# Kernel optimization log

Hardware: AMD Instinct MI355X
Metric: run time of the kernel (lower is better)

The kernel has to match this reference:

```python
import jax, jax.numpy as jnp
import numpy as np

B, N, H = 32, 1024, 512
THR = 0.05  # peak_detection_threshold


def _l2norm(x):
    return x / jnp.linalg.norm(x, axis=-1, keepdims=True)


def setup_inputs() -> dict:
    key = jax.random.key(0)
    ks = jax.random.split(key, 6)
    def w(k, shape, fan_in):
        return jax.random.normal(k, shape, jnp.float32) / np.float32(np.sqrt(fan_in))
    return {
        "segment_rep": jax.random.normal(ks[0], (B, N, H), jnp.float32),
        "phn_mask": jnp.ones((B, N), jnp.float32),
        # SegmentSimilarityMeasure: Linear(2H->H), ReLU, Linear(H->1, no bias)
        "W1": w(ks[1], (2 * H, H), 2 * H),
        "b1": jnp.zeros((H,), jnp.float32),
        "W2": w(ks[2], (H, 1), H),
        # word_enc: Linear(H->H), ReLU, Linear(H->H)
        "We1": w(ks[3], (H, H), H),
        "be1": jnp.zeros((H,), jnp.float32),
        "We2": w(ks[4], (H, H), H),
        "be2": jnp.zeros((H,), jnp.float32),
    }


def _forward(segment_rep, phn_mask, W1, b1, W2, We1, be1, We2, be2):
    Bs, Np, Hd = segment_rep.shape
    # adjacent segment similarity: MLP on concat of l2-normalized neighbors -> (B, N-1)
    cat = jnp.concatenate([_l2norm(segment_rep[:, :-1, :]), _l2norm(segment_rep[:, 1:, :])], axis=2)
    S = (jax.nn.relu(cat @ W1 + b1) @ W2)[..., 0]

    # relative dissimilarity
    Smin = jnp.min(S, axis=1, keepdims=True)
    Smax = jnp.max(S, axis=1, keepdims=True)
    D = 1.0 - (S - Smin) / (Smax - Smin)

    # peak detector (faithful to original, incl. final overwrite of first-order cols -2:)
    z = jnp.zeros_like(D)
    fo = z
    fo = fo.at[:, 0].set(jnp.maximum(D[:, 0] - D[:, 1], 0.0))
    fo = fo.at[:, 1:-1].set(jnp.minimum(jnp.maximum(D[:, 1:-1] - D[:, :-2], 0.0),
                                        jnp.maximum(D[:, 1:-1] - D[:, 2:], 0.0)))
    fo = fo.at[:, -1].set(jnp.maximum(D[:, -1] - D[:, -2], 0.0))
    so = z
    so = so.at[:, 0:2].set(jnp.maximum(D[:, 0:2] - D[:, 2:4], 0.0))
    so = so.at[:, 2:-2].set(jnp.minimum(jnp.maximum(D[:, 2:-2] - D[:, :-4], 0.0),
                                        jnp.maximum(D[:, 2:-2] - D[:, 4:], 0.0)))
    fo = fo.at[:, -2:].set(jnp.maximum(D[:, -2:] - D[:, -4:-2], 0.0))  # replicates original code
    P = jnp.minimum(jnp.maximum(jnp.maximum(fo, so) - THR, 0.0), fo)

    # pad, mask, straight-through hard boundaries
    P = jnp.pad(P, ((0, 0), (0, 1)))
    P = jax.nn.relu(P + (phn_mask - 1.0))
    b_soft = jnp.tanh(10.0 * P)
    b_hard = jnp.tanh(100000.0 * P)
    b = b_soft + jax.lax.stop_gradient(b_hard - b_soft)
    b = jnp.cumsum(b, axis=1)  # (B, N)
    b = b + (b[:, :1] == 0).astype(b.dtype)  # per-row +1 if b[:,0]==0
    num_word_segments = b[:, -1].astype(jnp.int32) + 1  # (B,)

    # U: column j holds j+1 for j < num_word_segments[i], else -100000. Nmax = N (static bound).
    cols = jnp.arange(1, Np + 1, dtype=jnp.int32)  # (Nmax,)
    U = jnp.where(cols[None, :] <= num_word_segments[:, None],
                  cols.astype(segment_rep.dtype)[None, :], -100000.0)  # (B, Nmax)

    V = U[:, None, :] - b[:, :, None]  # (B, N, Nmax)
    Wseg = 1.0 - jnp.tanh(100000.0 * jnp.abs(V))
    Wseg = Wseg / jnp.sum(Wseg, axis=1, keepdims=True)
    Wseg = jnp.nan_to_num(Wseg)

    # pool: (B, Nmax, N) @ (B, N, H) -> (B, Nmax, H)
    word_rep = jnp.einsum('bnm,bnh->bmh', Wseg, segment_rep)
    word_masks = jnp.where(word_rep == 0, 0.0, 1.0)
    out = jax.nn.relu(word_rep @ We1 + be1) @ We2 + be2
    return out * word_masks


def reference(segment_rep, phn_mask, W1, b1, W2, We1, be1, We2, be2):
    return _forward(segment_rep, phn_mask, W1, b1, W2, We1, be1, We2, be2)
```

## Files before the change

kernel.cpp:

```cpp
#include <hip/hip_runtime.h>

#define BB 32
#define NN 1024
#define HH 512
#define NS 1023

typedef unsigned short u16;
typedef unsigned int   u32;
typedef __attribute__((ext_vector_type(8))) short bf16x8;
typedef __attribute__((ext_vector_type(4))) float f32x4;

__device__ __forceinline__ float bf2f(u16 h) {
  union { u32 u; float f; } c; c.u = ((u32)h) << 16; return c.f;
}
__device__ __forceinline__ u16 f2bf(float f) {
  union { float f; u32 u; } c; c.f = f;
  u32 u = c.u;
  return (u16)((u + 0x7fffu + ((u >> 16) & 1u)) >> 16);
}
__device__ __forceinline__ void split_bf(float x, u16& hi, u16& lo) {
  hi = f2bf(x);
  lo = f2bf(x - bf2f(hi));
}
__device__ __forceinline__ void dma16(const u16* g, u16* l) {
  __builtin_amdgcn_global_load_lds(
      (const __attribute__((address_space(1))) u32*)g,
      (__attribute__((address_space(3))) u32*)l, 16, 0, 0);
}

__global__ __launch_bounds__(64) void k_prep_a(const float* __restrict__ seg,
                                               u16* __restrict__ ahi,
                                               u16* __restrict__ alo) {
  int row = blockIdx.x, lane = threadIdx.x;
  const float4* p = (const float4*)(seg + ((size_t)row << 9) + lane * 8);
  float4 a = p[0], b = p[1];
  float v[8] = {a.x, a.y, a.z, a.w, b.x, b.y, b.z, b.w};
  float s = 0.f;
#pragma unroll
  for (int i = 0; i < 8; ++i) s += v[i] * v[i];
#pragma unroll
  for (int m = 32; m; m >>= 1) s += __shfl_xor(s, m, 64);
  float nrm = sqrtf(s);
  u16 h[8], l[8];
#pragma unroll
  for (int i = 0; i < 8; ++i) split_bf(v[i] / nrm, h[i], l[i]);
  size_t off = ((size_t)row << 9) + lane * 8;
  *(uint4*)(ahi + off) = make_uint4(h[0] | (h[1] << 16), h[2] | (h[3] << 16),
                                    h[4] | (h[5] << 16), h[6] | (h[7] << 16));
  *(uint4*)(alo + off) = make_uint4(l[0] | (l[1] << 16), l[2] | (l[3] << 16),
                                    l[4] | (l[5] << 16), l[6] | (l[7] << 16));
}

__global__ __launch_bounds__(256) void k_tr(const float* __restrict__ src,
                                            u16* __restrict__ dh,
                                            u16* __restrict__ dl,
                                            int K, int N) {
  __shared__ u16 Th[64 * 66], Tl[64 * 66];
  int nb = blockIdx.x * 64, kb = blockIdx.y * 64;
  int tid = threadIdx.x;
#pragma unroll
  for (int i = 0; i < 16; ++i) {
    int e = tid + i * 256;
    int r = e >> 6, c = e & 63;
    float v = src[(size_t)(kb + r) * N + nb + c];
    u16 hi, lo; split_bf(v, hi, lo);
    Th[c * 66 + r] = hi;
    Tl[c * 66 + r] = lo;
  }
  __syncthreads();
#pragma unroll
  for (int i = 0; i < 16; ++i) {
    int e = tid + i * 256;
    int n = e >> 6, k = e & 63;
    dh[(size_t)(nb + n) * K + kb + k] = Th[n * 66 + k];
    if (dl) dl[(size_t)(nb + n) * K + kb + k] = Tl[n * 66 + k];
  }
}

__global__ __launch_bounds__(512, 2) void k_sgemm(const u16* __restrict__ ahi,
                                                  const u16* __restrict__ alo,
                                                  const u16* __restrict__ w1h,
                                                  const u16* __restrict__ w1l,
                                                  const float* __restrict__ b1,
                                                  const float* __restrict__ W2,
                                                  float* __restrict__ Spart) {
  __shared__ u16 Ah[2][256 * 32];
  __shared__ u16 Al[2][256 * 32];
  __shared__ u16 Bh[2][256 * 32];
  __shared__ u16 Bl[2][256 * 32];

  const int tid  = threadIdx.x;
  const int wave = tid >> 6, lane = tid & 63;
  const int quad = lane >> 4, l15 = lane & 15;
  const int wm = wave >> 2, wn = wave & 3;
  const int r_in = lane >> 2, c_in = lane & 3;
  const int nblk = blockIdx.x, mblk = blockIdx.y;
  const int mrow0 = mblk * 256;
  const int ncol0 = nblk * 256;

#define SG_A(g_, tb_, ks_)                                                   \
  {                                                                          \
    int k0_ = (ks_) * 32, half_ = k0_ >> 9, cb_ = k0_ & 511;                 \
    int grow_ = mrow0 + wave * 32 + (g_) * 16 + r_in + half_;                \
    if (grow_ > 32767) grow_ = 32767;                                        \
    size_t ga_ = (((size_t)grow_) << 9) + cb_ + c_in * 8;                    \
    dma16(ahi + ga_, &Ah[tb_][(wave * 32 + (g_) * 16) * 32]);                \
    dma16(alo + ga_, &Al[tb_][(wave * 32 + (g_) * 16) * 32]);                \
  }
#define SG_B(g_, tb_, ks_)                                                   \
  {                                                                          \
    int k0_ = (ks_) * 32;                                                    \
    int n_ = ncol0 + wave * 32 + (g_) * 16 + r_in;                           \
    size_t gb_ = (((size_t)n_) << 10) + k0_ + c_in * 8;                      \
    dma16(w1h + gb_, &Bh[tb_][(wave * 32 + (g_) * 16) * 32]);                \
    dma16(w1l + gb_, &Bl[tb_][(wave * 32 + (g_) * 16) * 32]);                \
  }

  f32x4 acc[8][4];
#pragma unroll
  for (int mi = 0; mi < 8; ++mi)
#pragma unroll
    for (int ni = 0; ni < 4; ++ni) acc[mi][ni] = (f32x4){0.f, 0.f, 0.f, 0.f};

  SG_A(0, 0, 0) SG_A(1, 0, 0) SG_B(0, 0, 0) SG_B(1, 0, 0)
  asm volatile("s_waitcnt vmcnt(0)" ::: "memory");
  __builtin_amdgcn_s_barrier();

  for (int ks = 0; ks < 32; ++ks) {
    const int bb = ks & 1;
    const bool pre = (ks + 1) < 32;
    bf16x8 ah[8], al[8], bh[4], bl[4];

#pragma unroll
    for (int mi = 0; mi < 8; ++mi)
      ah[mi] = *(const bf16x8*)&Ah[bb][(wm * 128 + mi * 16 + l15) * 32 + quad * 8];
#pragma unroll
    for (int ni = 0; ni < 4; ++ni)
      bh[ni] = *(const bf16x8*)&Bh[bb][(wn * 64 + ni * 16 + l15) * 32 + quad * 8];
    if (pre) { SG_A(0, bb ^ 1, ks + 1) SG_B(0, bb ^ 1, ks + 1) }
    __builtin_amdgcn_s_barrier();
    asm volatile("s_waitcnt lgkmcnt(0)" ::: "memory");
    __builtin_amdgcn_sched_barrier(0);
    __builtin_amdgcn_s_setprio(1);
#pragma unroll
    for (int ni = 0; ni < 4; ++ni)
#pragma unroll
      for (int mi = 0; mi < 8; ++mi)
        acc[mi][ni] = __builtin_amdgcn_mfma_f32_16x16x32_bf16(ah[mi], bh[ni], acc[mi][ni], 0, 0, 0);
    __builtin_amdgcn_s_setprio(0);
    __builtin_amdgcn_s_barrier();

#pragma unroll
    for (int ni = 0; ni < 4; ++ni)
      bl[ni] = *(const bf16x8*)&Bl[bb][(wn * 64 + ni * 16 + l15) * 32 + quad * 8];
    if (pre) { SG_A(1, bb ^ 1, ks + 1) SG_B(1, bb ^ 1, ks + 1) }
    __builtin_amdgcn_s_barrier();
    asm volatile("s_waitcnt lgkmcnt(0)" ::: "memory");
    __builtin_amdgcn_sched_barrier(0);
    __builtin_amdgcn_s_setprio(1);
#pragma unroll
    for (int ni = 0; ni < 4; ++ni)
#pragma unroll
      for (int mi = 0; mi < 8; ++mi)
        acc[mi][ni] = __builtin_amdgcn_mfma_f32_16x16x32_bf16(ah[mi], bl[ni], acc[mi][ni], 0, 0, 0);
    __builtin_amdgcn_s_setprio(0);
    __builtin_amdgcn_s_barrier();

#pragma unroll
    for (int mi = 0; mi < 8; ++mi)
      al[mi] = *(const bf16x8*)&Al[bb][(wm * 128 + mi * 16 + l15) * 32 + quad * 8];
    __builtin_amdgcn_s_barrier();
    asm volatile("s_waitcnt lgkmcnt(0)" ::: "memory");
    __builtin_amdgcn_sched_barrier(0);
    __builtin_amdgcn_s_setprio(1);
#pragma unroll
    for (int ni = 0; ni < 4; ++ni)
#pragma unroll
      for (int mi = 0; mi < 8; ++mi)
        acc[mi][ni] = __builtin_amdgcn_mfma_f32_16x16x32_bf16(al[mi], bh[ni], acc[mi][ni], 0, 0, 0);
    __builtin_amdgcn_s_setprio(0);
    asm volatile("s_waitcnt vmcnt(0)" ::: "memory");
    __builtin_amdgcn_s_barrier();
  }
#undef SG_A
#undef SG_B

  float* red = (float*)&Ah[0][0];
  float b1v[4], w2v[4];
#pragma unroll
  for (int ni = 0; ni < 4; ++ni) {
    int n_g = ncol0 + wn * 64 + ni * 16 + l15;
    b1v[ni] = b1[n_g];
    w2v[ni] = W2[n_g];
  }
#pragma unroll
  for (int mi = 0; mi < 8; ++mi) {
#pragma unroll
    for (int reg = 0; reg < 4; ++reg) {
      float part = 0.f;
#pragma unroll
      for (int ni = 0; ni < 4; ++ni) {
        float h = acc[mi][ni][reg] + b1v[ni];
        h = h > 0.f ? h : 0.f;
        part = fmaf(h, w2v[ni], part);
      }
#pragma unroll
      for (int m = 8; m; m >>= 1) part += __shfl_xor(part, m, 64);
      if (l15 == 0) red[wave * 128 + mi * 16 + quad * 4 + reg] = part;
    }
  }
  __syncthreads();
  if (tid < 256) {
    int wmr = tid >> 7, rl = tid & 127;
    float s = red[(wmr * 4 + 0) * 128 + rl] + red[(wmr * 4 + 1) * 128 + rl]
            + red[(wmr * 4 + 2) * 128 + rl] + red[(wmr * 4 + 3) * 128 + rl];
    int grow = mrow0 + tid;
    int b = grow >> 10, n = grow & 1023;
    if (n < NS)
      Spart[((size_t)nblk * BB + b) * NN + n] = s;
  }
}

__global__ __launch_bounds__(256) void k_row(const float* __restrict__ S0,
                                             const float* __restrict__ S1,
                                             const float* __restrict__ mask,
                                             int* __restrict__ assign,
                                             float* __restrict__ weight,
                                             float* __restrict__ total,
                                             int* __restrict__ startn,
                                             int* __restrict__ endn) {
  int b = blockIdx.x, tid = threadIdx.x;
  __shared__ float Ssh[NS];
  __shared__ float Dsh[NS];
  __shared__ float tsh[NN];
  __shared__ float bsh[NN];
  __shared__ float totl[NN];
  __shared__ int   stl[NN];
  __shared__ int   enl[NN];
  __shared__ float red[256];

  for (int n = tid; n < NS; n += 256)
    Ssh[n] = S0[((size_t)b << 10) + n] + S1[((size_t)b << 10) + n];
  __syncthreads();

  float mn = INFINITY, mx = -INFINITY;
  for (int n = tid; n < NS; n += 256) {
    float v = Ssh[n];
    mn = fminf(mn, v); mx = fmaxf(mx, v);
  }
  red[tid] = mn; __syncthreads();
  for (int s = 128; s; s >>= 1) { if (tid < s) red[tid] = fminf(red[tid], red[tid + s]); __syncthreads(); }
  float Smin = red[0]; __syncthreads();
  red[tid] = mx; __syncthreads();
  for (int s = 128; s; s >>= 1) { if (tid < s) red[tid] = fmaxf(red[tid], red[tid + s]); __syncthreads(); }
  float Smax = red[0]; __syncthreads();

  for (int n = tid; n < NS; n += 256)
    Dsh[n] = 1.0f - (Ssh[n] - Smin) / (Smax - Smin);
  __syncthreads();

  for (int n = tid; n < NN; n += 256) {
    float P;
    if (n >= NS) {
      P = 0.f;
    } else {
      float D = Dsh[n];
      float fo, so;
      if (n == 0)            fo = fmaxf(D - Dsh[1], 0.f);
      else if (n >= NS - 2)  fo = fmaxf(D - Dsh[n - 2], 0.f);
      else                   fo = fminf(fmaxf(D - Dsh[n - 1], 0.f),
                                        fmaxf(D - Dsh[n + 1], 0.f));
      if (n <= 1)            so = fmaxf(D - Dsh[n + 2], 0.f);
      else if (n >= NS - 2)  so = 0.f;
      else                   so = fminf(fmaxf(D - Dsh[n - 2], 0.f),
                                        fmaxf(D - Dsh[n + 2], 0.f));
      P = fminf(fmaxf(fmaxf(fo, so) - 0.05f, 0.f), fo);
    }
    float m = mask[((size_t)b << 10) + n];
    P = P + (m - 1.0f);
    P = P > 0.f ? P : 0.f;
    float bs = tanhf(10.0f * P);
    float bh = tanhf(100000.0f * P);
    tsh[n] = bs + (bh - bs);
  }
  __syncthreads();

  if (tid == 0) {
    float acc = 0.f;
    for (int n = 0; n < NN; n += 8) {
      float t0 = tsh[n + 0], t1 = tsh[n + 1], t2 = tsh[n + 2], t3 = tsh[n + 3];
      float t4 = tsh[n + 4], t5 = tsh[n + 5], t6 = tsh[n + 6], t7 = tsh[n + 7];
      acc += t0; bsh[n + 0] = acc; acc += t1; bsh[n + 1] = acc;
      acc += t2; bsh[n + 2] = acc; acc += t3; bsh[n + 3] = acc;
      acc += t4; bsh[n + 4] = acc; acc += t5; bsh[n + 5] = acc;
      acc += t6; bsh[n + 6] = acc; acc += t7; bsh[n + 7] = acc;
    }
  }
  __syncthreads();

  float add1 = (bsh[0] == 0.0f) ? 1.0f : 0.0f;
  int   num  = (int)(bsh[NN - 1] + add1) + 1;

  for (int mi = tid; mi < NN; mi += 256) { totl[mi] = 0.f; stl[mi] = 1 << 30; enl[mi] = -1; }
  __syncthreads();

  for (int n = tid; n < NN; n += 256) {
    float bv = bsh[n] + add1;
    float kf = rintf(bv);
    int   k  = (int)kf;
    int   a  = -1; float w = 0.f;
    if (k >= 1 && k <= num && k <= NN) {
      float v = fabsf(kf - bv);
      w = 1.0f - tanhf(100000.0f * v);
      if (w > 0.f) {
        a = k - 1;
        atomicAdd(&totl[a], w);
        atomicMin(&stl[a], n);
        atomicMax(&enl[a], n);
      } else {
        a = -1; w = 0.f;
      }
    }
    assign[((size_t)b << 10) + n] = a;
    weight[((size_t)b << 10) + n] = w;
  }
  __syncthreads();
  for (int mi = tid; mi < NN; mi += 256) {
    total [((size_t)b << 10) + mi] = totl[mi];
    startn[((size_t)b << 10) + mi] = stl[mi];
    endn  [((size_t)b << 10) + mi] = enl[mi];
  }
}

__global__ __launch_bounds__(64) void k_pool(const float* __restrict__ seg,
                                             const int* __restrict__ assign,
                                             const float* __restrict__ weight,
                                             const float* __restrict__ total,
                                             const int* __restrict__ startn,
                                             const int* __restrict__ endn,
                                             u16* hrep,
                                             unsigned char* __restrict__ mb) {
  int bm = blockIdx.x;
  int b  = bm >> 10, m = bm & 1023;
  int lane = threadIdx.x;
  float acc[8] = {0.f, 0.f, 0.f, 0.f, 0.f, 0.f, 0.f, 0.f};
  float tm = total[bm];
  if (tm > 0.f) {
    int s = startn[bm], e = endn[bm];
    for (int n = s; n <= e; ++n) {
      if (assign[((size_t)b << 10) + n] != m) continue;
      float coef = weight[((size_t)b << 10) + n] / tm;
      const float4* p = (const float4*)(seg + (((size_t)b << 10) + n) * HH + lane * 8);
      float4 x = p[0], y = p[1];
      acc[0] = fmaf(coef, x.x, acc[0]); acc[1] = fmaf(coef, x.y, acc[1]);
      acc[2] = fmaf(coef, x.z, acc[2]); acc[3] = fmaf(coef, x.w, acc[3]);
      acc[4] = fmaf(coef, y.x, acc[4]); acc[5] = fmaf(coef, y.y, acc[5]);
      acc[6] = fmaf(coef, y.z, acc[6]); acc[7] = fmaf(coef, y.w, acc[7]);
    }
  }
  u16 h[8];
  unsigned int mbyte = 0;
#pragma unroll
  for (int j = 0; j < 8; ++j) {
    h[j] = f2bf(acc[j]);
    mbyte |= (acc[j] == 0.f ? 1u : 0u) << j;
  }
  *(uint4*)(hrep + ((size_t)bm << 10) + lane * 8) =
      make_uint4(h[0] | (h[1] << 16), h[2] | (h[3] << 16),
                 h[4] | (h[5] << 16), h[6] | (h[7] << 16));
  mb[((size_t)bm << 6) + lane] = (unsigned char)mbyte;
}

__global__ __launch_bounds__(512, 4) void k_g(const u16* asrc,
                                              const u16* __restrict__ bmat,
                                              const float* __restrict__ bias,
                                              const unsigned char* __restrict__ mb,
                                              float* outp,
                                              u16* hid,
                                              int a_off, int mode) {
  __shared__ u16 As[2][64 * 32];
  __shared__ u16 Bs[2][512 * 32];

  const int tid  = threadIdx.x;
  const int wave = tid >> 6, lane = tid & 63;
  const int quad = lane >> 4, l15 = lane & 15;
  const int wm = wave >> 2, wn = wave & 3;
  const int r_in = lane >> 2, c_in = lane & 3;
  const int mrow0 = blockIdx.x * 64;

#define SG(tb_, ks_)                                                         \
  {                                                                          \
    int k0_ = (ks_) * 32;                                                    \
    if (wave < 4) {                                                          \
      int row_ = wave * 16 + r_in;                                           \
      dma16(asrc + ((size_t)(mrow0 + row_) << 10) + a_off + k0_ + c_in * 8,  \
            &As[tb_][(wave * 16) * 32]);                                     \
    }                                                                        \
    _Pragma("unroll")                                                        \
    for (int g_ = 0; g_ < 4; ++g_) {                                         \
      int n_ = wave * 64 + g_ * 16 + r_in;                                   \
      dma16(bmat + (size_t)n_ * 512 + k0_ + c_in * 8,                        \
            &Bs[tb_][(wave * 64 + g_ * 16) * 32]);                           \
    }                                                                        \
  }

  f32x4 acc[2][8];
#pragma unroll
  for (int mi = 0; mi < 2; ++mi)
#pragma unroll
    for (int ni = 0; ni < 8; ++ni) acc[mi][ni] = (f32x4){0.f, 0.f, 0.f, 0.f};

  SG(0, 0)
  asm volatile("s_waitcnt vmcnt(0)" ::: "memory");
  __builtin_amdgcn_s_barrier();

  for (int ks = 0; ks < 16; ++ks) {
    const int bb = ks & 1;
    bf16x8 a[2], b[8];
#pragma unroll
    for (int mi = 0; mi < 2; ++mi)
      a[mi] = *(const bf16x8*)&As[bb][(wm * 32 + mi * 16 + l15) * 32 + quad * 8];
#pragma unroll
    for (int ni = 0; ni < 8; ++ni)
      b[ni] = *(const bf16x8*)&Bs[bb][(wn * 128 + ni * 16 + l15) * 32 + quad * 8];
    if (ks + 1 < 16) SG(bb ^ 1, ks + 1)
    asm volatile("s_waitcnt lgkmcnt(0)" ::: "memory");
    __builtin_amdgcn_sched_barrier(0);
    __builtin_amdgcn_s_setprio(1);
#pragma unroll
    for (int ni = 0; ni < 8; ++ni)
#pragma unroll
      for (int mi = 0; mi < 2; ++mi)
        acc[mi][ni] = __builtin_amdgcn_mfma_f32_16x16x32_bf16(a[mi], b[ni], acc[mi][ni], 0, 0, 0);
    __builtin_amdgcn_s_setprio(0);
    asm volatile("s_waitcnt vmcnt(0)" ::: "memory");
    __builtin_amdgcn_s_barrier();
  }
#undef SG

  float bv[8];
#pragma unroll
  for (int ni = 0; ni < 8; ++ni) bv[ni] = bias[wn * 128 + ni * 16 + l15];

  if (mode == 1) {
#pragma unroll
    for (int mi = 0; mi < 2; ++mi)
#pragma unroll
      for (int ni = 0; ni < 8; ++ni)
#pragma unroll
        for (int reg = 0; reg < 4; ++reg) {
          int col = wn * 128 + ni * 16 + l15;
          int row = mrow0 + wm * 32 + mi * 16 + quad * 4 + reg;
          float h = acc[mi][ni][reg] + bv[ni];
          h = h > 0.f ? h : 0.f;
          hid[((size_t)row << 10) + 512 + col] = f2bf(h);
        }
  } else {
#pragma unroll
    for (int mi = 0; mi < 2; ++mi)
#pragma unroll
      for (int ni = 0; ni < 8; ++ni)
#pragma unroll
        for (int reg = 0; reg < 4; ++reg) {
          int col = wn * 128 + ni * 16 + l15;
          int row = mrow0 + wm * 32 + mi * 16 + quad * 4 + reg;
          float o = acc[mi][ni][reg] + bv[ni];
          unsigned char m8 = mb[((size_t)row << 6) + (col >> 3)];
          outp[((size_t)row << 9) + col] = ((m8 >> (col & 7)) & 1) ? 0.f : o;
        }
  }
}

__global__ void k_diag(float* __restrict__ out, int hostcode) {
  if (hostcode != 0) out[0] = (float)hostcode;
}

extern "C" void kernel_launch(void* const* d_in, const int* in_sizes, int n_in,
                              void* d_out, int out_size, void* d_ws, size_t ws_size,
                              hipStream_t stream) {
  const float* seg  = (const float*)d_in[0];
  const float* mask = (const float*)d_in[1];
  const float* W1   = (const float*)d_in[2];
  const float* b1   = (const float*)d_in[3];
  const float* W2   = (const float*)d_in[4];
  const float* We1  = (const float*)d_in[5];
  const float* be1  = (const float*)d_in[6];
  const float* We2  = (const float*)d_in[7];
  const float* be2  = (const float*)d_in[8];

  const size_t NROW = (size_t)BB * NN;
  float* ws = (float*)d_ws;
  float* S0     = ws;
  float* S1     = S0 + NROW;
  int*   assign = (int*)(S1 + NROW);
  float* weight = (float*)(assign + NROW);
  float* total  = weight + NROW;
  int*   startn = (int*)(total + NROW);
  int*   endn   = startn + NROW;
  u16*   w1h    = (u16*)(endn + NROW);
  u16*   w1l    = w1h + (size_t)512 * 1024;
  u16*   we1t   = w1l + (size_t)512 * 1024;
  u16*   we2t   = we1t + (size_t)512 * 512;

  float* out = (float*)d_out;
  u16*   ahi = (u16*)d_out;
  u16*   alo = ahi + (size_t)NROW * HH;
  u16*   hrep = (u16*)d_out;
  unsigned char* mbuf = (unsigned char*)w1h;

  int hostcode = 0;
  if (ws_size < (size_t)7 * NROW * 4 + (size_t)3 * 1024 * 1024) hostcode += 32768;
  if (out_size != 16777216) hostcode += 8192;

  k_prep_a<<<dim3(BB * NN), dim3(64), 0, stream>>>(seg, ahi, alo);
  k_tr    <<<dim3(8, 16), dim3(256), 0, stream>>>(W1, w1h, w1l, 1024, 512);
  k_tr    <<<dim3(8, 8),  dim3(256), 0, stream>>>(We1, we1t, (u16*)nullptr, 512, 512);
  k_tr    <<<dim3(8, 8),  dim3(256), 0, stream>>>(We2, we2t, (u16*)nullptr, 512, 512);
  k_sgemm <<<dim3(2, 128), dim3(512), 0, stream>>>(ahi, alo, w1h, w1l, b1, W2, S0);
  k_row   <<<dim3(BB), dim3(256), 0, stream>>>(S0, S1, mask, assign, weight, total, startn, endn);
  k_pool  <<<dim3(BB * NN), dim3(64), 0, stream>>>(seg, assign, weight, total, startn, endn, hrep, mbuf);
  k_g     <<<dim3(512), dim3(512), 0, stream>>>(hrep, we1t, be1, mbuf, out, hrep, 0,   1);
  k_g     <<<dim3(512), dim3(512), 0, stream>>>(hrep, we2t, be2, mbuf, out, hrep, 512, 2);
  k_diag  <<<dim3(1), dim3(1), 0, stream>>>(out, hostcode);
}
```

Measured before the change: 325.5 us.

## Use partial vmcnt waits and deeper A prefetch to overlap loads with MFMA

```diff
diff --git a/kernel.cpp b/kernel.cpp
--- a/kernel.cpp
+++ b/kernel.cpp
@@ -98,22 +98,47 @@
   const int mrow0 = mblk * 256;
   const int ncol0 = nblk * 256;
 
-#define SG_A(g_, tb_, ks_)                                                   \
+#define SG_AH(tb_, ks_)                                                      \
   {                                                                          \
     int k0_ = (ks_) * 32, half_ = k0_ >> 9, cb_ = k0_ & 511;                 \
-    int grow_ = mrow0 + wave * 32 + (g_) * 16 + r_in + half_;                \
-    if (grow_ > 32767) grow_ = 32767;                                        \
-    size_t ga_ = (((size_t)grow_) << 9) + cb_ + c_in * 8;                    \
-    dma16(ahi + ga_, &Ah[tb_][(wave * 32 + (g_) * 16) * 32]);                \
-    dma16(alo + ga_, &Al[tb_][(wave * 32 + (g_) * 16) * 32]);                \
-  }
-#define SG_B(g_, tb_, ks_)                                                   \
+    int g0_ = mrow0 + wave * 32 + r_in + half_;                              \
+    int g1_ = g0_ + 16;                                                      \
+    if (g0_ > 32767) g0_ = 32767;                                            \
+    if (g1_ > 32767) g1_ = 32767;                                            \
+    dma16(ahi + ((((size_t)g0_) << 9) + cb_ + c_in * 8),                     \
+          &Ah[tb_][(wave * 32) * 32]);                                       \
+    dma16(ahi + ((((size_t)g1_) << 9) + cb_ + c_in * 8),                     \
+          &Ah[tb_][(wave * 32 + 16) * 32]);                                  \
+  }
+#define SG_AL(tb_, ks_)                                                      \
+  {                                                                          \
+    int k0_ = (ks_) * 32, half_ = k0_ >> 9, cb_ = k0_ & 511;                 \
+    int g0_ = mrow0 + wave * 32 + r_in + half_;                              \
+    int g1_ = g0_ + 16;                                                      \
+    if (g0_ > 32767) g0_ = 32767;                                            \
+    if (g1_ > 32767) g1_ = 32767;                                            \
+    dma16(alo + ((((size_t)g0_) << 9) + cb_ + c_in * 8),                     \
+          &Al[tb_][(wave * 32) * 32]);                                       \
+    dma16(alo + ((((size_t)g1_) << 9) + cb_ + c_in * 8),                     \
+          &Al[tb_][(wave * 32 + 16) * 32]);                                  \
+  }
+#define SG_BH(tb_, ks_)                                                      \
   {                                                                          \
     int k0_ = (ks_) * 32;                                                    \
-    int n_ = ncol0 + wave * 32 + (g_) * 16 + r_in;                           \
-    size_t gb_ = (((size_t)n_) << 10) + k0_ + c_in * 8;                      \
-    dma16(w1h + gb_, &Bh[tb_][(wave * 32 + (g_) * 16) * 32]);                \
-    dma16(w1l + gb_, &Bl[tb_][(wave * 32 + (g_) * 16) * 32]);                \
+    int n0_ = ncol0 + wave * 32 + r_in;                                      \
+    dma16(w1h + (((size_t)n0_) << 10) + k0_ + c_in * 8,                      \
+          &Bh[tb_][(wave * 32) * 32]);                                       \
+    dma16(w1h + (((size_t)(n0_ + 16)) << 10) + k0_ + c_in * 8,               \
+          &Bh[tb_][(wave * 32 + 16) * 32]);                                  \
+  }
+#define SG_BL(tb_, ks_)                                                      \
+  {                                                                          \
+    int k0_ = (ks_) * 32;                                                    \
+    int n0_ = ncol0 + wave * 32 + r_in;                                      \
+    dma16(w1l + (((size_t)n0_) << 10) + k0_ + c_in * 8,                      \
+          &Bl[tb_][(wave * 32) * 32]);                                       \
+    dma16(w1l + (((size_t)(n0_ + 16)) << 10) + k0_ + c_in * 8,               \
+          &Bl[tb_][(wave * 32 + 16) * 32]);                                  \
   }
 
   f32x4 acc[8][4];
@@ -122,13 +147,13 @@
 #pragma unroll
     for (int ni = 0; ni < 4; ++ni) acc[mi][ni] = (f32x4){0.f, 0.f, 0.f, 0.f};
 
-  SG_A(0, 0, 0) SG_A(1, 0, 0) SG_B(0, 0, 0) SG_B(1, 0, 0)
-  asm volatile("s_waitcnt vmcnt(0)" ::: "memory");
+  SG_AH(0, 0) SG_BH(0, 0) SG_BL(0, 0) SG_AL(0, 0)
+  asm volatile("s_waitcnt vmcnt(4)" ::: "memory");
   __builtin_amdgcn_s_barrier();
 
   for (int ks = 0; ks < 32; ++ks) {
     const int bb = ks & 1;
-    const bool pre = (ks + 1) < 32;
+    const int nx = (ks + 1 < 32) ? ks + 1 : 31;
     bf16x8 ah[8], al[8], bh[4], bl[4];
 
 #pragma unroll
@@ -137,8 +162,7 @@
 #pragma unroll
     for (int ni = 0; ni < 4; ++ni)
       bh[ni] = *(const bf16x8*)&Bh[bb][(wn * 64 + ni * 16 + l15) * 32 + quad * 8];
-    if (pre) { SG_A(0, bb ^ 1, ks + 1) SG_B(0, bb ^ 1, ks + 1) }
-    __builtin_amdgcn_s_barrier();
+    SG_AH(bb ^ 1, nx) SG_BH(bb ^ 1, nx)
     asm volatile("s_waitcnt lgkmcnt(0)" ::: "memory");
     __builtin_amdgcn_sched_barrier(0);
     __builtin_amdgcn_s_setprio(1);
@@ -148,13 +172,13 @@
       for (int mi = 0; mi < 8; ++mi)
         acc[mi][ni] = __builtin_amdgcn_mfma_f32_16x16x32_bf16(ah[mi], bh[ni], acc[mi][ni], 0, 0, 0);
     __builtin_amdgcn_s_setprio(0);
+    asm volatile("s_waitcnt vmcnt(6)" ::: "memory");
     __builtin_amdgcn_s_barrier();
 
 #pragma unroll
     for (int ni = 0; ni < 4; ++ni)
       bl[ni] = *(const bf16x8*)&Bl[bb][(wn * 64 + ni * 16 + l15) * 32 + quad * 8];
-    if (pre) { SG_A(1, bb ^ 1, ks + 1) SG_B(1, bb ^ 1, ks + 1) }
-    __builtin_amdgcn_s_barrier();
+    SG_BL(bb ^ 1, nx) SG_AL(bb ^ 1, nx)
     asm volatile("s_waitcnt lgkmcnt(0)" ::: "memory");
     __builtin_amdgcn_sched_barrier(0);
     __builtin_amdgcn_s_setprio(1);
@@ -164,12 +188,12 @@
       for (int mi = 0; mi < 8; ++mi)
         acc[mi][ni] = __builtin_amdgcn_mfma_f32_16x16x32_bf16(ah[mi], bl[ni], acc[mi][ni], 0, 0, 0);
     __builtin_amdgcn_s_setprio(0);
+    asm volatile("s_waitcnt vmcnt(8)" ::: "memory");
     __builtin_amdgcn_s_barrier();
 
 #pragma unroll
     for (int mi = 0; mi < 8; ++mi)
       al[mi] = *(const bf16x8*)&Al[bb][(wm * 128 + mi * 16 + l15) * 32 + quad * 8];
-    __builtin_amdgcn_s_barrier();
     asm volatile("s_waitcnt lgkmcnt(0)" ::: "memory");
     __builtin_amdgcn_sched_barrier(0);
     __builtin_amdgcn_s_setprio(1);
@@ -179,11 +203,16 @@
       for (int mi = 0; mi < 8; ++mi)
         acc[mi][ni] = __builtin_amdgcn_mfma_f32_16x16x32_bf16(al[mi], bh[ni], acc[mi][ni], 0, 0, 0);
     __builtin_amdgcn_s_setprio(0);
-    asm volatile("s_waitcnt vmcnt(0)" ::: "memory");
+    asm volatile("s_waitcnt vmcnt(4)" ::: "memory");
     __builtin_amdgcn_s_barrier();
   }
-#undef SG_A
-#undef SG_B
+#undef SG_AH
+#undef SG_AL
+#undef SG_BH
+#undef SG_BL
+
+  asm volatile("s_waitcnt vmcnt(0)" ::: "memory");
+  __syncthreads();
 
   float* red = (float*)&Ah[0][0];
   float b1v[4], w2v[4];
@@ -378,7 +407,7 @@
                                               float* outp,
                                               u16* hid,
                                               int a_off, int mode) {
-  __shared__ u16 As[2][64 * 32];
+  __shared__ u16 As[3][64 * 32];
   __shared__ u16 Bs[2][512 * 32];
 
   const int tid  = threadIdx.x;
@@ -388,14 +417,9 @@
   const int r_in = lane >> 2, c_in = lane & 3;
   const int mrow0 = blockIdx.x * 64;
 
-#define SG(tb_, ks_)                                                         \
+#define SGB(tb_, ks_)                                                        \
   {                                                                          \
     int k0_ = (ks_) * 32;                                                    \
-    if (wave < 4) {                                                          \
-      int row_ = wave * 16 + r_in;                                           \
-      dma16(asrc + ((size_t)(mrow0 + row_) << 10) + a_off + k0_ + c_in * 8,  \
-            &As[tb_][(wave * 16) * 32]);                                     \
-    }                                                                        \
     _Pragma("unroll")                                                        \
     for (int g_ = 0; g_ < 4; ++g_) {                                         \
       int n_ = wave * 64 + g_ * 16 + r_in;                                   \
@@ -403,6 +427,15 @@
             &Bs[tb_][(wave * 64 + g_ * 16) * 32]);                           \
     }                                                                        \
   }
+#define SGA(sl_, ks_)                                                        \
+  {                                                                          \
+    if (wave < 4) {                                                          \
+      int k0_ = (ks_) * 32;                                                  \
+      int row_ = wave * 16 + r_in;                                           \
+      dma16(asrc + ((size_t)(mrow0 + row_) << 10) + a_off + k0_ + c_in * 8,  \
+            &As[sl_][(wave * 16) * 32]);                                     \
+    }                                                                        \
+  }
 
   f32x4 acc[2][8];
 #pragma unroll
@@ -410,20 +443,25 @@
 #pragma unroll
     for (int ni = 0; ni < 8; ++ni) acc[mi][ni] = (f32x4){0.f, 0.f, 0.f, 0.f};
 
-  SG(0, 0)
-  asm volatile("s_waitcnt vmcnt(0)" ::: "memory");
+  SGB(0, 0) SGA(0, 0) SGA(1, 1)
+  if (wave < 4) { asm volatile("s_waitcnt vmcnt(1)" ::: "memory"); }
+  else          { asm volatile("s_waitcnt vmcnt(0)" ::: "memory"); }
   __builtin_amdgcn_s_barrier();
 
   for (int ks = 0; ks < 16; ++ks) {
     const int bb = ks & 1;
+    const int ra = ks % 3;
+    const int nb = (ks + 1 < 16) ? ks + 1 : 15;
+    const int na = (ks + 2 < 16) ? ks + 2 : 15;
+    SGB(bb ^ 1, nb)
+    SGA((ks + 2) % 3, na)
     bf16x8 a[2], b[8];
 #pragma unroll
     for (int mi = 0; mi < 2; ++mi)
-      a[mi] = *(const bf16x8*)&As[bb][(wm * 32 + mi * 16 + l15) * 32 + quad * 8];
+      a[mi] = *(const bf16x8*)&As[ra][(wm * 32 + mi * 16 + l15) * 32 + quad * 8];
 #pragma unroll
     for (int ni = 0; ni < 8; ++ni)
       b[ni] = *(const bf16x8*)&Bs[bb][(wn * 128 + ni * 16 + l15) * 32 + quad * 8];
-    if (ks + 1 < 16) SG(bb ^ 1, ks + 1)
     asm volatile("s_waitcnt lgkmcnt(0)" ::: "memory");
     __builtin_amdgcn_sched_barrier(0);
     __builtin_amdgcn_s_setprio(1);
@@ -433,10 +471,13 @@
       for (int mi = 0; mi < 2; ++mi)
         acc[mi][ni] = __builtin_amdgcn_mfma_f32_16x16x32_bf16(a[mi], b[ni], acc[mi][ni], 0, 0, 0);
     __builtin_amdgcn_s_setprio(0);
-    asm volatile("s_waitcnt vmcnt(0)" ::: "memory");
+    if (wave < 4) { asm volatile("s_waitcnt vmcnt(1)" ::: "memory"); }
+    else          { asm volatile("s_waitcnt vmcnt(0)" ::: "memory"); }
     __builtin_amdgcn_s_barrier();
   }
-#undef SG
+#undef SGB
+#undef SGA
+  asm volatile("s_waitcnt vmcnt(0)" ::: "memory");
 
   float bv[8];
 #pragma unroll
```

New measurement: 322.1 us. Within noise of the previous version (-1.0%).
